# Performance work log

Hardware: AMD Instinct MI355X
Metric: run time of the kernel (lower is better)

Reference implementation:

```python
import jax, jax.numpy as jnp
import numpy as np

B, C, H, W = 8, 256, 64, 64
CQK = C // 8  # query/key channels = 32


def setup_inputs() -> dict:
    key = jax.random.key(0)
    ks = jax.random.split(key, 9)
    s_in = 1.0 / np.sqrt(C)  # conv2d default init scale (kernel_size=1)
    x = jax.random.normal(ks[0], (B, C, H, W), dtype=jnp.float32)
    Wq = jax.random.uniform(ks[1], (CQK, C), jnp.float32, -s_in, s_in)
    bq = jax.random.uniform(ks[2], (CQK,), jnp.float32, -s_in, s_in)
    Wk = jax.random.uniform(ks[3], (CQK, C), jnp.float32, -s_in, s_in)
    bk = jax.random.uniform(ks[4], (CQK,), jnp.float32, -s_in, s_in)
    Wv = jax.random.uniform(ks[5], (C, C), jnp.float32, -s_in, s_in)
    bv = jax.random.uniform(ks[6], (C,), jnp.float32, -s_in, s_in)
    Wf = jax.random.uniform(ks[7], (C, C), jnp.float32, -s_in, s_in)
    bf = jax.random.uniform(ks[8], (C,), jnp.float32, -s_in, s_in)
    return {"x": x, "Wq": Wq, "bq": bq, "Wk": Wk, "bk": bk,
            "Wv": Wv, "bv": bv, "Wf": Wf, "bf": bf}


def reference(x, Wq, bq, Wk, bk, Wv, bv, Wf, bf):
    b, c, h, w = x.shape
    n = h * w
    xf = x.reshape(b, c, n)  # [B, C, N]  (1x1 conv == channel matmul)
    q = jnp.einsum('oc,bcn->bon', Wq, xf) + bq[None, :, None]  # [B, C/8, N]
    k = jnp.einsum('oc,bcn->bon', Wk, xf) + bk[None, :, None]  # [B, C/8, N]
    v = jnp.einsum('oc,bcn->bon', Wv, xf) + bv[None, :, None]  # [B, C, N]
    # energy[b,i,j] = sum_c q[b,c,i] * k[b,c,j]; no scaling (matches source)
    energy = jnp.einsum('bci,bcj->bij', q, k)  # [B, N, N]
    attn = jax.nn.softmax(energy, axis=-1)
    # out[b,c,i] = sum_j v[b,c,j] * attn[b,i,j]
    out = jnp.einsum('bcj,bij->bci', v, attn)  # [B, C, N]
    out = jnp.einsum('oc,bcn->bon', Wf, out) + bf[None, :, None]
    return out.reshape(b, c, h, w)
```

## Files before the change

kernel.cpp:

```cpp
#include <hip/hip_runtime.h>
#include <hip/hip_bf16.h>

#define BATCH 8
#define CCH   256
#define NPOS  4096
#define CQK   32

typedef __attribute__((ext_vector_type(8))) short short8;
typedef __attribute__((ext_vector_type(4))) float f32x4;

__device__ inline unsigned short f2b(float f) {
    __hip_bfloat16 h = __float2bfloat16(f);
    return *reinterpret_cast<unsigned short*>(&h);
}

__device__ inline size_t qk_addr(int b, int n, int c) {
    return ((((size_t)b * 256 + (n >> 4)) * 4 + (c >> 3)) * 16 + (n & 15)) * 8 + (c & 7);
}
__device__ inline size_t xt_addr(int b, int n, int c) {
    return (((size_t)b * 256 + (n >> 4)) * 8 + (c >> 5)) * 512
           + (((c >> 3) & 3) * 16 + (n & 15)) * 8 + (c & 7);
}
__device__ inline size_t v_addr(int b, int c, int j) {
    return (((((size_t)b * 128 + (j >> 5)) * 16 + (c >> 4)) * 4 + ((j >> 3) & 3)) * 16 + (c & 15)) * 8 + (j & 7);
}
__device__ inline size_t wsw_addr(int og, int c, int ol) {
    return ((size_t)(og * 8 + (c >> 5))) * 512 + (((c >> 3) & 3) * 16 + ol) * 8 + (c & 7);
}

__global__ __launch_bounds__(256, 2)
void prep_kernel(const float* __restrict__ x,
                 const float* __restrict__ Wq, const float* __restrict__ Wk,
                 const float* __restrict__ Wv, const float* __restrict__ Wf,
                 unsigned short* __restrict__ xt, unsigned short* __restrict__ wsw)
{
    const int bid = blockIdx.x;
    const int t   = threadIdx.x;
    if (bid < 2048) {
        __shared__ float xl[64 * 65];
        const int b   = bid >> 8;
        const int rem = bid & 255;
        const int n0  = (rem & 63) * 64;
        const int c0  = (rem >> 6) * 64;
        #pragma unroll
        for (int ch = 0; ch < 4; ++ch) {
            int f  = t + ch * 256;
            int cl = f >> 4, n4 = (f & 15) * 4;
            float4 v = *(const float4*)(x + (size_t)(b * 256 + c0 + cl) * 4096 + n0 + n4);
            xl[cl * 65 + n4 + 0] = v.x;
            xl[cl * 65 + n4 + 1] = v.y;
            xl[cl * 65 + n4 + 2] = v.z;
            xl[cl * 65 + n4 + 3] = v.w;
        }
        __syncthreads();
        #pragma unroll
        for (int e = 0; e < 2; ++e) {
            int f  = t + e * 256;
            int nl = f >> 3, c8 = (f & 7) * 8;
            short8 s;
            #pragma unroll
            for (int j = 0; j < 8; ++j)
                ((unsigned short*)&s)[j] = f2b(xl[(c8 + j) * 65 + nl]);
            *(short8*)(xt + xt_addr(b, n0 + nl, c0 + c8)) = s;
        }
    } else {
        const int og = bid - 2048;
        const float* src; int orow;
        if (og < 2)       { src = Wq; orow = og * 16; }
        else if (og < 4)  { src = Wk; orow = (og - 2) * 16; }
        else if (og < 20) { src = Wv; orow = (og - 4) * 16; }
        else              { src = Wf; orow = (og - 20) * 16; }
        #pragma unroll
        for (int e = 0; e < 16; ++e) {
            int idx = t + e * 256;
            int ol = idx >> 8, c = idx & 255;
            wsw[wsw_addr(og, c, ol)] = f2b(src[(orow + ol) * 256 + c]);
        }
    }
}

__global__ __launch_bounds__(256, 2)
void qkv_kernel(const unsigned short* __restrict__ xt,
                const unsigned short* __restrict__ wsw,
                const float* __restrict__ bq, const float* __restrict__ bk,
                const float* __restrict__ bv,
                unsigned short* __restrict__ qb, unsigned short* __restrict__ kb,
                unsigned short* __restrict__ vb)
{
    const int nt = blockIdx.x;
    const int ot = blockIdx.y;
    const int b  = blockIdx.z;
    const int t  = threadIdx.x;
    const int w  = t >> 6;
    const int q  = (t >> 4) & 3;
    const int ln = t & 15;
    const int lofs = (q * 16 + ln) * 8;

    if (ot == 0) {
        const int og   = w;
        const int cb16 = (w & 1) * 16;
        short8 af[8];
        #pragma unroll
        for (int kk = 0; kk < 8; ++kk)
            af[kk] = *(const short8*)(wsw + (size_t)(og * 8 + kk) * 512 + lofs);
        const float* bias = (w < 2) ? bq : bk;
        const float b0 = bias[cb16 + q * 4 + 0];
        const float b1 = bias[cb16 + q * 4 + 1];
        const float b2 = bias[cb16 + q * 4 + 2];
        const float b3 = bias[cb16 + q * 4 + 3];
        unsigned short* dst = (w < 2) ? qb : kb;
        #pragma unroll
        for (int nq = 0; nq < 4; ++nq) {
            f32x4 acc = {b0, b1, b2, b3};
            const size_t xbase = (size_t)((b * 256 + nt * 4 + nq) * 8) * 512;
            #pragma unroll
            for (int kk = 0; kk < 8; ++kk) {
                short8 bfr = *(const short8*)(xt + xbase + (size_t)kk * 512 + lofs);
                acc = __builtin_amdgcn_mfma_f32_16x16x32_bf16(af[kk], bfr, acc, 0, 0, 0);
            }
            ushort4 s = {f2b(acc[0]), f2b(acc[1]), f2b(acc[2]), f2b(acc[3])};
            *(ushort4*)(dst + qk_addr(b, nt * 64 + nq * 16 + ln, cb16 + q * 4)) = s;
        }
    } else {
        const int cv0 = (ot - 1) * 64;
        short8 af[8];
        const size_t xbase = (size_t)((b * 256 + nt * 4 + w) * 8) * 512;
        #pragma unroll
        for (int kk = 0; kk < 8; ++kk)
            af[kk] = *(const short8*)(xt + xbase + (size_t)kk * 512 + lofs);
        const int jbase = nt * 64 + w * 16;
        #pragma unroll
        for (int oq = 0; oq < 4; ++oq) {
            const int c = cv0 + oq * 16 + ln;
            const float bb = bv[c];
            f32x4 acc = {bb, bb, bb, bb};
            const int og = 4 + (ot - 1) * 4 + oq;
            #pragma unroll
            for (int kk = 0; kk < 8; ++kk) {
                short8 bfr = *(const short8*)(wsw + (size_t)(og * 8 + kk) * 512 + lofs);
                acc = __builtin_amdgcn_mfma_f32_16x16x32_bf16(af[kk], bfr, acc, 0, 0, 0);
            }
            ushort4 s = {f2b(acc[0]), f2b(acc[1]), f2b(acc[2]), f2b(acc[3])};
            *(ushort4*)(vb + v_addr(b, c, jbase + q * 4)) = s;
        }
    }
}

__global__ __launch_bounds__(256, 2)
void attn_kernel(const unsigned short* __restrict__ qb,
                 const unsigned short* __restrict__ kb,
                 const unsigned short* __restrict__ vb,
                 unsigned short* __restrict__ obb)
{
    __shared__ unsigned short plds[2][64][72];
    __shared__ float lred[64];

    const int bid  = blockIdx.x;
    const int b    = bid & 7;
    const int i0   = (bid >> 3) * 64;
    const int t    = threadIdx.x;
    const int w    = t >> 6;
    const int lane = t & 63;
    const int quad = lane >> 4;
    const int ln   = lane & 15;

    const int ibase = i0 + w * 16;
    const int lofs  = (quad * 16 + ln) * 8;

    const short8 qfrag = *(const short8*)(qb + (((size_t)b * 256 + (ibase >> 4)) * 512) + lofs);

    f32x4 acc[4][4];
    #pragma unroll
    for (int it = 0; it < 4; ++it)
        #pragma unroll
        for (int cc = 0; cc < 4; ++cc) acc[it][cc] = (f32x4){0.f, 0.f, 0.f, 0.f};
    float accl[4] = {0.f, 0.f, 0.f, 0.f};

    const unsigned short* kbase = kb + (size_t)b * 256 * 512;
    const unsigned short* vbase = vb + (size_t)b * 128 * 8192;

    int pb = 0;
    for (int j0 = 0; j0 < 4096; j0 += 64, pb ^= 1) {
        f32x4 s[4];
        #pragma unroll
        for (int jc = 0; jc < 4; ++jc) {
            short8 kfrag = *(const short8*)(kbase + ((size_t)((j0 >> 4) + jc) * 512) + lofs);
            s[jc] = __builtin_amdgcn_mfma_f32_16x16x32_bf16(qfrag, kfrag,
                     (f32x4){0.f, 0.f, 0.f, 0.f}, 0, 0, 0);
        }
        #pragma unroll
        for (int jc = 0; jc < 4; ++jc) {
            #pragma unroll
            for (int r = 0; r < 4; ++r) {
                float p = __expf(s[jc][r]);
                accl[r] += p;
                plds[pb][w * 16 + quad * 4 + r][jc * 16 + ln] = f2b(p);
            }
        }
        __syncthreads();
        const unsigned short* vt0 = vbase + (size_t)(j0 >> 5) * 8192;
        short8 vf[4][2];
        #pragma unroll
        for (int cc = 0; cc < 4; ++cc) {
            vf[cc][0] = *(const short8*)(vt0 + (w * 4 + cc) * 512 + lofs);
            vf[cc][1] = *(const short8*)(vt0 + 8192 + (w * 4 + cc) * 512 + lofs);
        }
        #pragma unroll
        for (int it = 0; it < 4; ++it) {
            const short8 pf0 = *(const short8*)&plds[pb][it * 16 + ln][quad * 8];
            const short8 pf1 = *(const short8*)&plds[pb][it * 16 + ln][32 + quad * 8];
            #pragma unroll
            for (int cc = 0; cc < 4; ++cc) {
                acc[it][cc] = __builtin_amdgcn_mfma_f32_16x16x32_bf16(pf0, vf[cc][0], acc[it][cc], 0, 0, 0);
                acc[it][cc] = __builtin_amdgcn_mfma_f32_16x16x32_bf16(pf1, vf[cc][1], acc[it][cc], 0, 0, 0);
            }
        }
    }

    #pragma unroll
    for (int r = 0; r < 4; ++r) {
        float v = accl[r];
        v += __shfl_xor(v, 1, 16);
        v += __shfl_xor(v, 2, 16);
        v += __shfl_xor(v, 4, 16);
        v += __shfl_xor(v, 8, 16);
        if (ln == 0) lred[w * 16 + quad * 4 + r] = v;
    }
    __syncthreads();

    #pragma unroll
    for (int it = 0; it < 4; ++it) {
        float linv[4];
        #pragma unroll
        for (int r = 0; r < 4; ++r) linv[r] = 1.f / lred[it * 16 + quad * 4 + r];
        #pragma unroll
        for (int cc = 0; cc < 4; ++cc) {
            const int c = w * 64 + cc * 16 + ln;
            #pragma unroll
            for (int r = 0; r < 4; ++r) {
                const int i = i0 + it * 16 + quad * 4 + r;
                obb[xt_addr(b, i, c)] = f2b(acc[it][cc][r] * linv[r]);
            }
        }
    }
}

__global__ __launch_bounds__(256, 2)
void proj_kernel(const unsigned short* __restrict__ obb,
                 const unsigned short* __restrict__ wsw,
                 const float* __restrict__ bfb, float* __restrict__ out)
{
    const int it = blockIdx.x;
    const int ot = blockIdx.y;
    const int b  = blockIdx.z;
    const int t  = threadIdx.x;
    const int w  = t >> 6;
    const int q  = (t >> 4) & 3;
    const int ln = t & 15;
    const int lofs = (q * 16 + ln) * 8;

    short8 af[8];
    const size_t abase = (size_t)((b * 256 + it * 4 + w) * 8) * 512;
    #pragma unroll
    for (int kk = 0; kk < 8; ++kk)
        af[kk] = *(const short8*)(obb + abase + (size_t)kk * 512 + lofs);

    const int ibase = it * 64 + w * 16;
    #pragma unroll
    for (int oq = 0; oq < 4; ++oq) {
        f32x4 acc = {0.f, 0.f, 0.f, 0.f};
        const int og = 20 + ot * 4 + oq;
        #pragma unroll
        for (int kk = 0; kk < 8; ++kk) {
            short8 bfr = *(const short8*)(wsw + (size_t)(og * 8 + kk) * 512 + lofs);
            acc = __builtin_amdgcn_mfma_f32_16x16x32_bf16(af[kk], bfr, acc, 0, 0, 0);
        }
        const int o = ot * 64 + oq * 16 + ln;
        const float bias = bfb[o];
        float4 s = {acc[0] + bias, acc[1] + bias, acc[2] + bias, acc[3] + bias};
        *(float4*)(out + (size_t)(b * 256 + o) * 4096 + ibase + q * 4) = s;
    }
}

extern "C" void kernel_launch(void* const* d_in, const int* in_sizes, int n_in,
                              void* d_out, int out_size, void* d_ws, size_t ws_size,
                              hipStream_t stream)
{
    const float* x  = (const float*)d_in[0];
    const float* Wq = (const float*)d_in[1];
    const float* bq = (const float*)d_in[2];
    const float* Wk = (const float*)d_in[3];
    const float* bk = (const float*)d_in[4];
    const float* Wv = (const float*)d_in[5];
    const float* bv = (const float*)d_in[6];
    const float* Wf = (const float*)d_in[7];
    const float* bf = (const float*)d_in[8];
    float* out = (float*)d_out;

    unsigned short* xt  = (unsigned short*)d_ws;
    unsigned short* qb  = xt + (size_t)BATCH * NPOS * CCH;
    unsigned short* kb  = qb + (size_t)BATCH * NPOS * CQK;
    unsigned short* vb  = kb + (size_t)BATCH * NPOS * CQK;
    unsigned short* wsw = vb + (size_t)BATCH * CCH * NPOS;
    unsigned short* obb = xt;

    prep_kernel<<<2048 + 36, 256, 0, stream>>>(x, Wq, Wk, Wv, Wf, xt, wsw);
    qkv_kernel<<<dim3(64, 5, 8), 256, 0, stream>>>(xt, wsw, bq, bk, bv, qb, kb, vb);
    attn_kernel<<<512, 256, 0, stream>>>(qb, kb, vb, obb);
    proj_kernel<<<dim3(64, 4, 8), 256, 0, stream>>>(obb, wsw, bf, out);
}
```

Before: 225.6 us.

## Fuse x transpose into QKV kernel and software-pipeline K/V loads in attention

```diff
diff --git a/kernel.cpp b/kernel.cpp
--- a/kernel.cpp
+++ b/kernel.cpp
@@ -28,121 +28,94 @@
     return ((size_t)(og * 8 + (c >> 5))) * 512 + (((c >> 3) & 3) * 16 + ol) * 8 + (c & 7);
 }
 
-__global__ __launch_bounds__(256, 2)
-void prep_kernel(const float* __restrict__ x,
-                 const float* __restrict__ Wq, const float* __restrict__ Wk,
-                 const float* __restrict__ Wv, const float* __restrict__ Wf,
-                 unsigned short* __restrict__ xt, unsigned short* __restrict__ wsw)
-{
-    const int bid = blockIdx.x;
-    const int t   = threadIdx.x;
-    if (bid < 2048) {
-        __shared__ float xl[64 * 65];
-        const int b   = bid >> 8;
-        const int rem = bid & 255;
-        const int n0  = (rem & 63) * 64;
-        const int c0  = (rem >> 6) * 64;
-        #pragma unroll
-        for (int ch = 0; ch < 4; ++ch) {
-            int f  = t + ch * 256;
-            int cl = f >> 4, n4 = (f & 15) * 4;
-            float4 v = *(const float4*)(x + (size_t)(b * 256 + c0 + cl) * 4096 + n0 + n4);
-            xl[cl * 65 + n4 + 0] = v.x;
-            xl[cl * 65 + n4 + 1] = v.y;
-            xl[cl * 65 + n4 + 2] = v.z;
-            xl[cl * 65 + n4 + 3] = v.w;
-        }
-        __syncthreads();
-        #pragma unroll
-        for (int e = 0; e < 2; ++e) {
-            int f  = t + e * 256;
-            int nl = f >> 3, c8 = (f & 7) * 8;
-            short8 s;
-            #pragma unroll
-            for (int j = 0; j < 8; ++j)
-                ((unsigned short*)&s)[j] = f2b(xl[(c8 + j) * 65 + nl]);
-            *(short8*)(xt + xt_addr(b, n0 + nl, c0 + c8)) = s;
-        }
-    } else {
-        const int og = bid - 2048;
-        const float* src; int orow;
-        if (og < 2)       { src = Wq; orow = og * 16; }
-        else if (og < 4)  { src = Wk; orow = (og - 2) * 16; }
-        else if (og < 20) { src = Wv; orow = (og - 4) * 16; }
-        else              { src = Wf; orow = (og - 20) * 16; }
-        #pragma unroll
-        for (int e = 0; e < 16; ++e) {
-            int idx = t + e * 256;
-            int ol = idx >> 8, c = idx & 255;
-            wsw[wsw_addr(og, c, ol)] = f2b(src[(orow + ol) * 256 + c]);
-        }
-    }
-}
-
-__global__ __launch_bounds__(256, 2)
-void qkv_kernel(const unsigned short* __restrict__ xt,
+__global__ __launch_bounds__(256, 4)
+void wprep_kernel(const float* __restrict__ Wq, const float* __restrict__ Wk,
+                  const float* __restrict__ Wv, const float* __restrict__ Wf,
+                  unsigned short* __restrict__ wsw)
+{
+    const int og = blockIdx.x;
+    const int t  = threadIdx.x;
+    const float* src; int orow;
+    if (og < 2)       { src = Wq; orow = og * 16; }
+    else if (og < 4)  { src = Wk; orow = (og - 2) * 16; }
+    else if (og < 20) { src = Wv; orow = (og - 4) * 16; }
+    else              { src = Wf; orow = (og - 20) * 16; }
+    #pragma unroll
+    for (int e = 0; e < 16; ++e) {
+        int idx = t + e * 256;
+        int ol = idx >> 8, c = idx & 255;
+        wsw[wsw_addr(og, c, ol)] = f2b(src[(orow + ol) * 256 + c]);
+    }
+}
+
+__global__ __launch_bounds__(256, 3)
+void qkv_kernel(const float* __restrict__ x,
                 const unsigned short* __restrict__ wsw,
                 const float* __restrict__ bq, const float* __restrict__ bk,
                 const float* __restrict__ bv,
                 unsigned short* __restrict__ qb, unsigned short* __restrict__ kb,
                 unsigned short* __restrict__ vb)
 {
+    __shared__ unsigned short xl[32 * 512];
+
     const int nt = blockIdx.x;
-    const int ot = blockIdx.y;
-    const int b  = blockIdx.z;
+    const int b  = blockIdx.y;
     const int t  = threadIdx.x;
-    const int w  = t >> 6;
-    const int q  = (t >> 4) & 3;
-    const int ln = t & 15;
-    const int lofs = (q * 16 + ln) * 8;
-
-    if (ot == 0) {
-        const int og   = w;
-        const int cb16 = (w & 1) * 16;
-        short8 af[8];
-        #pragma unroll
-        for (int kk = 0; kk < 8; ++kk)
-            af[kk] = *(const short8*)(wsw + (size_t)(og * 8 + kk) * 512 + lofs);
-        const float* bias = (w < 2) ? bq : bk;
-        const float b0 = bias[cb16 + q * 4 + 0];
-        const float b1 = bias[cb16 + q * 4 + 1];
-        const float b2 = bias[cb16 + q * 4 + 2];
-        const float b3 = bias[cb16 + q * 4 + 3];
-        unsigned short* dst = (w < 2) ? qb : kb;
-        #pragma unroll
-        for (int nq = 0; nq < 4; ++nq) {
-            f32x4 acc = {b0, b1, b2, b3};
-            const size_t xbase = (size_t)((b * 256 + nt * 4 + nq) * 8) * 512;
-            #pragma unroll
-            for (int kk = 0; kk < 8; ++kk) {
-                short8 bfr = *(const short8*)(xt + xbase + (size_t)kk * 512 + lofs);
-                acc = __builtin_amdgcn_mfma_f32_16x16x32_bf16(af[kk], bfr, acc, 0, 0, 0);
-            }
-            ushort4 s = {f2b(acc[0]), f2b(acc[1]), f2b(acc[2]), f2b(acc[3])};
-            *(ushort4*)(dst + qk_addr(b, nt * 64 + nq * 16 + ln, cb16 + q * 4)) = s;
-        }
-    } else {
-        const int cv0 = (ot - 1) * 64;
-        short8 af[8];
-        const size_t xbase = (size_t)((b * 256 + nt * 4 + w) * 8) * 512;
-        #pragma unroll
-        for (int kk = 0; kk < 8; ++kk)
-            af[kk] = *(const short8*)(xt + xbase + (size_t)kk * 512 + lofs);
-        const int jbase = nt * 64 + w * 16;
-        #pragma unroll
-        for (int oq = 0; oq < 4; ++oq) {
-            const int c = cv0 + oq * 16 + ln;
-            const float bb = bv[c];
-            f32x4 acc = {bb, bb, bb, bb};
-            const int og = 4 + (ot - 1) * 4 + oq;
-            #pragma unroll
-            for (int kk = 0; kk < 8; ++kk) {
-                short8 bfr = *(const short8*)(wsw + (size_t)(og * 8 + kk) * 512 + lofs);
-                acc = __builtin_amdgcn_mfma_f32_16x16x32_bf16(af[kk], bfr, acc, 0, 0, 0);
-            }
-            ushort4 s = {f2b(acc[0]), f2b(acc[1]), f2b(acc[2]), f2b(acc[3])};
-            *(ushort4*)(vb + v_addr(b, c, jbase + q * 4)) = s;
-        }
+    const int w    = t >> 6;
+    const int quad = (t >> 4) & 3;
+    const int ln   = t & 15;
+    const int lofs = (quad * 16 + ln) * 8;
+    const int n0 = nt * 64;
+
+    #pragma unroll
+    for (int ch = 0; ch < 16; ++ch) {
+        int idx = t + ch * 256;
+        int c   = idx >> 4;
+        int n4  = (idx & 15) * 4;
+        float4 v = *(const float4*)(x + (size_t)(b * 256 + c) * 4096 + n0 + n4);
+        #pragma unroll
+        for (int jj = 0; jj < 4; ++jj) {
+            int nl  = n4 + jj;
+            int off = ((nl >> 4) * 8 + (c >> 5)) * 512
+                    + (((c >> 3) & 3) * 16 + (nl & 15)) * 8 + (c & 7);
+            xl[off] = f2b(((const float*)&v)[jj]);
+        }
+    }
+    __syncthreads();
+
+    short8 xf[8];
+    #pragma unroll
+    for (int kk = 0; kk < 8; ++kk)
+        xf[kk] = *(const short8*)&xl[(w * 8 + kk) * 512 + lofs];
+
+    #pragma unroll
+    for (int og = 0; og < 4; ++og) {
+        const float* bias = (og < 2) ? bq : bk;
+        const int cb16 = (og & 1) * 16;
+        f32x4 acc = {bias[cb16 + quad * 4 + 0], bias[cb16 + quad * 4 + 1],
+                     bias[cb16 + quad * 4 + 2], bias[cb16 + quad * 4 + 3]};
+        #pragma unroll
+        for (int kk = 0; kk < 8; ++kk) {
+            short8 af = *(const short8*)(wsw + (size_t)(og * 8 + kk) * 512 + lofs);
+            acc = __builtin_amdgcn_mfma_f32_16x16x32_bf16(af, xf[kk], acc, 0, 0, 0);
+        }
+        ushort4 s = {f2b(acc[0]), f2b(acc[1]), f2b(acc[2]), f2b(acc[3])};
+        unsigned short* dst = (og < 2) ? qb : kb;
+        *(ushort4*)(dst + qk_addr(b, n0 + w * 16 + ln, cb16 + quad * 4)) = s;
+    }
+
+    #pragma unroll
+    for (int og = 4; og < 20; ++og) {
+        const int c = (og - 4) * 16 + ln;
+        const float bb = bv[c];
+        f32x4 acc = {bb, bb, bb, bb};
+        #pragma unroll
+        for (int kk = 0; kk < 8; ++kk) {
+            short8 bfr = *(const short8*)(wsw + (size_t)(og * 8 + kk) * 512 + lofs);
+            acc = __builtin_amdgcn_mfma_f32_16x16x32_bf16(xf[kk], bfr, acc, 0, 0, 0);
+        }
+        ushort4 s = {f2b(acc[0]), f2b(acc[1]), f2b(acc[2]), f2b(acc[3])};
+        *(ushort4*)(vb + v_addr(b, c, n0 + w * 16 + quad * 4)) = s;
     }
 }
 
@@ -164,67 +137,79 @@
     const int quad = lane >> 4;
     const int ln   = lane & 15;
 
-    const int ibase = i0 + w * 16;
-    const int lofs  = (quad * 16 + ln) * 8;
-
-    const short8 qfrag = *(const short8*)(qb + (((size_t)b * 256 + (ibase >> 4)) * 512) + lofs);
+    const int lofs = (quad * 16 + ln) * 8;
+
+    const short8 qfrag = *(const short8*)(qb + (((size_t)b * 256 + ((i0 >> 4) + w)) * 512) + lofs);
 
     f32x4 acc[4][4];
     #pragma unroll
     for (int it = 0; it < 4; ++it)
         #pragma unroll
         for (int cc = 0; cc < 4; ++cc) acc[it][cc] = (f32x4){0.f, 0.f, 0.f, 0.f};
-    float accl[4] = {0.f, 0.f, 0.f, 0.f};
+    float accl = 0.f;
 
     const unsigned short* kbase = kb + (size_t)b * 256 * 512;
     const unsigned short* vbase = vb + (size_t)b * 128 * 8192;
 
-    int pb = 0;
-    for (int j0 = 0; j0 < 4096; j0 += 64, pb ^= 1) {
-        f32x4 s[4];
-        #pragma unroll
-        for (int jc = 0; jc < 4; ++jc) {
-            short8 kfrag = *(const short8*)(kbase + ((size_t)((j0 >> 4) + jc) * 512) + lofs);
-            s[jc] = __builtin_amdgcn_mfma_f32_16x16x32_bf16(qfrag, kfrag,
-                     (f32x4){0.f, 0.f, 0.f, 0.f}, 0, 0, 0);
-        }
-        #pragma unroll
-        for (int jc = 0; jc < 4; ++jc) {
-            #pragma unroll
-            for (int r = 0; r < 4; ++r) {
-                float p = __expf(s[jc][r]);
-                accl[r] += p;
-                plds[pb][w * 16 + quad * 4 + r][jc * 16 + ln] = f2b(p);
-            }
-        }
-        __syncthreads();
-        const unsigned short* vt0 = vbase + (size_t)(j0 >> 5) * 8192;
-        short8 vf[4][2];
-        #pragma unroll
-        for (int cc = 0; cc < 4; ++cc) {
-            vf[cc][0] = *(const short8*)(vt0 + (w * 4 + cc) * 512 + lofs);
-            vf[cc][1] = *(const short8*)(vt0 + 8192 + (w * 4 + cc) * 512 + lofs);
-        }
-        #pragma unroll
-        for (int it = 0; it < 4; ++it) {
-            const short8 pf0 = *(const short8*)&plds[pb][it * 16 + ln][quad * 8];
-            const short8 pf1 = *(const short8*)&plds[pb][it * 16 + ln][32 + quad * 8];
+    short8 kf[2][4], vf[2][4][2];
+    #pragma unroll
+    for (int jc = 0; jc < 4; ++jc)
+        kf[0][jc] = *(const short8*)(kbase + (size_t)jc * 512 + lofs);
+    #pragma unroll
+    for (int cc = 0; cc < 4; ++cc) {
+        vf[0][cc][0] = *(const short8*)(vbase + (w * 4 + cc) * 512 + lofs);
+        vf[0][cc][1] = *(const short8*)(vbase + 8192 + (w * 4 + cc) * 512 + lofs);
+    }
+
+    for (int j0 = 0; j0 < 4096; j0 += 128) {
+        #pragma unroll
+        for (int u = 0; u < 2; ++u) {
+            const int jnxt = (j0 + u * 64 + 64) & 4095;
+            #pragma unroll
+            for (int jc = 0; jc < 4; ++jc)
+                kf[u ^ 1][jc] = *(const short8*)(kbase + (size_t)((jnxt >> 4) + jc) * 512 + lofs);
+            const unsigned short* vtn = vbase + (size_t)(jnxt >> 5) * 8192;
             #pragma unroll
             for (int cc = 0; cc < 4; ++cc) {
-                acc[it][cc] = __builtin_amdgcn_mfma_f32_16x16x32_bf16(pf0, vf[cc][0], acc[it][cc], 0, 0, 0);
-                acc[it][cc] = __builtin_amdgcn_mfma_f32_16x16x32_bf16(pf1, vf[cc][1], acc[it][cc], 0, 0, 0);
-            }
-        }
-    }
-
-    #pragma unroll
-    for (int r = 0; r < 4; ++r) {
-        float v = accl[r];
-        v += __shfl_xor(v, 1, 16);
-        v += __shfl_xor(v, 2, 16);
-        v += __shfl_xor(v, 4, 16);
-        v += __shfl_xor(v, 8, 16);
-        if (ln == 0) lred[w * 16 + quad * 4 + r] = v;
+                vf[u ^ 1][cc][0] = *(const short8*)(vtn + (w * 4 + cc) * 512 + lofs);
+                vf[u ^ 1][cc][1] = *(const short8*)(vtn + 8192 + (w * 4 + cc) * 512 + lofs);
+            }
+            f32x4 s[4];
+            #pragma unroll
+            for (int jc = 0; jc < 4; ++jc)
+                s[jc] = __builtin_amdgcn_mfma_f32_16x16x32_bf16(kf[u][jc], qfrag,
+                         (f32x4){0.f, 0.f, 0.f, 0.f}, 0, 0, 0);
+            #pragma unroll
+            for (int jc = 0; jc < 4; ++jc) {
+                float p0 = __expf(s[jc][0]);
+                float p1 = __expf(s[jc][1]);
+                float p2 = __expf(s[jc][2]);
+                float p3 = __expf(s[jc][3]);
+                accl += (p0 + p1) + (p2 + p3);
+                uint2 uu;
+                uu.x = (unsigned)f2b(p0) | ((unsigned)f2b(p1) << 16);
+                uu.y = (unsigned)f2b(p2) | ((unsigned)f2b(p3) << 16);
+                *(uint2*)&plds[u][w * 16 + ln][jc * 16 + quad * 4] = uu;
+            }
+            __syncthreads();
+            #pragma unroll
+            for (int it = 0; it < 4; ++it) {
+                const short8 pf0 = *(const short8*)&plds[u][it * 16 + ln][quad * 8];
+                const short8 pf1 = *(const short8*)&plds[u][it * 16 + ln][32 + quad * 8];
+                #pragma unroll
+                for (int cc = 0; cc < 4; ++cc) {
+                    acc[it][cc] = __builtin_amdgcn_mfma_f32_16x16x32_bf16(pf0, vf[u][cc][0], acc[it][cc], 0, 0, 0);
+                    acc[it][cc] = __builtin_amdgcn_mfma_f32_16x16x32_bf16(pf1, vf[u][cc][1], acc[it][cc], 0, 0, 0);
+                }
+            }
+        }
+    }
+
+    {
+        float v = accl;
+        v += __shfl_xor(v, 16, 64);
+        v += __shfl_xor(v, 32, 64);
+        if (quad == 0) lred[w * 16 + ln] = v;
     }
     __syncthreads();
 
@@ -245,7 +230,7 @@
     }
 }
 
-__global__ __launch_bounds__(256, 2)
+__global__ __launch_bounds__(256, 4)
 void proj_kernel(const unsigned short* __restrict__ obb,
                  const unsigned short* __restrict__ wsw,
                  const float* __restrict__ bfb, float* __restrict__ out)
@@ -297,15 +282,14 @@
     const float* bf = (const float*)d_in[8];
     float* out = (float*)d_out;
 
-    unsigned short* xt  = (unsigned short*)d_ws;
-    unsigned short* qb  = xt + (size_t)BATCH * NPOS * CCH;
+    unsigned short* qb  = (unsigned short*)d_ws;
     unsigned short* kb  = qb + (size_t)BATCH * NPOS * CQK;
     unsigned short* vb  = kb + (size_t)BATCH * NPOS * CQK;
     unsigned short* wsw = vb + (size_t)BATCH * CCH * NPOS;
-    unsigned short* obb = xt;
-
-    prep_kernel<<<2048 + 36, 256, 0, stream>>>(x, Wq, Wk, Wv, Wf, xt, wsw);
-    qkv_kernel<<<dim3(64, 5, 8), 256, 0, stream>>>(xt, wsw, bq, bk, bv, qb, kb, vb);
+    unsigned short* obb = wsw + (size_t)36 * 8 * 512;
+
+    wprep_kernel<<<36, 256, 0, stream>>>(Wq, Wk, Wv, Wf, wsw);
+    qkv_kernel<<<dim3(64, 8), 256, 0, stream>>>(x, wsw, bq, bk, bv, qb, kb, vb);
     attn_kernel<<<512, 256, 0, stream>>>(qb, kb, vb, obb);
     proj_kernel<<<dim3(64, 4, 8), 256, 0, stream>>>(obb, wsw, bf, out);
 }
```

Result: slower. 231.7 us (+2.7%).
